# Kernel optimization log

Measured on AMD Instinct MI355X. Metric: run time of the kernel, lower is better.

Reference implementation:

```python
import jax, jax.numpy as jnp
import numpy as np

WS = 4          # window size per axis
HEADS = 3
HEAD_DIM = 32
DIM = 96
DISP = WS // 2  # displacement for shifted windows


def _make_mask(axis):
    # (w^3, w^3) additive mask, -inf across the wrap-around boundary on `axis`
    m = np.zeros((WS, WS, WS, WS, WS, WS), dtype=np.float32)
    d = DISP
    if axis == 0:
        m[-d:, :, :, :-d, :, :] = -np.inf
        m[:-d, :, :, -d:, :, :] = -np.inf
    elif axis == 1:
        m[:, -d:, :, :, :-d, :] = -np.inf
        m[:, :-d, :, :, -d:, :] = -np.inf
    else:
        m[:, :, -d:, :, :, :-d] = -np.inf
        m[:, :, :-d, :, :, -d:] = -np.inf
    return jnp.asarray(m.reshape(WS**3, WS**3))


def setup_inputs() -> dict:
    key = jax.random.key(0)
    k1, k2, k3, k4 = jax.random.split(key, 4)
    inner = HEADS * HEAD_DIM
    x = jax.random.normal(k1, (1, 64, 64, 64, DIM), dtype=jnp.float32)
    w_qkv = jax.random.normal(k2, (3 * inner, DIM), dtype=jnp.float32) * 0.02
    w_out = jax.random.normal(k3, (DIM, inner), dtype=jnp.float32) * 0.02
    b_out = jax.random.normal(k4, (DIM,), dtype=jnp.float32) * 0.02
    return {
        'x': x, 'w_qkv': w_qkv, 'w_out': w_out, 'b_out': b_out,
        'x_mask': _make_mask(0), 'y_mask': _make_mask(1), 'z_mask': _make_mask(2),
    }


def _forward(x, w_qkv, w_out, b_out, x_mask, y_mask, z_mask):
    scale = HEAD_DIM ** -0.5
    b, nx, ny, nz, _ = x.shape
    nwx, nwy, nwz = nx // WS, ny // WS, nz // WS
    seq = WS ** 3
    # cyclic shift by -displacement
    x = jnp.roll(x, shift=(-DISP, -DISP, -DISP), axis=(1, 2, 3))
    qkv = jnp.einsum('bxyzc,oc->bxyzo', x, w_qkv)
    q, k, v = jnp.split(qkv, 3, axis=-1)

    def win(t):  # -> (b, h, n_windows, seq, d)
        t = t.reshape(b, nwx, WS, nwy, WS, nwz, WS, HEADS, HEAD_DIM)
        t = t.transpose(0, 7, 1, 3, 5, 2, 4, 6, 8)
        return t.reshape(b, HEADS, nwx * nwy * nwz, seq, HEAD_DIM)

    q, k, v = win(q), win(k), win(v)
    dots = jnp.einsum('bhwid,bhwjd->bhwij', q, k) * scale

    # shifted-window masking (faithful to original einops relabeling, incl.
    # the final mislabeled rearrange which permutes the window grid)
    d = dots.reshape(b, HEADS, nwx, nwy, nwz, seq, seq)
    d = d.transpose(0, 1, 3, 4, 2, 5, 6)          # (b,h,ny,nz,nx,i,j)
    d = d.at[:, :, :, :, -1].add(x_mask)
    d = d.transpose(0, 1, 4, 3, 2, 5, 6)          # (b,h,nx,nz,ny,i,j)
    d = d.at[:, :, :, :, -1].add(y_mask)
    d = d.transpose(0, 1, 2, 4, 3, 5, 6)          # (b,h,nx,ny,nz,i,j)
    d = d.transpose(0, 1, 4, 2, 3, 5, 6)          # original's final rearrange bug
    dots = d.reshape(b, HEADS, nwx * nwy * nwz, seq, seq)

    attn = jax.nn.softmax(dots, axis=-1)
    out = jnp.einsum('bhwij,bhwjd->bhwid', attn, v)
    # un-window
    out = out.reshape(b, HEADS, nwx, nwy, nwz, WS, WS, WS, HEAD_DIM)
    out = out.transpose(0, 2, 5, 3, 6, 4, 7, 1, 8).reshape(b, nx, ny, nz, HEADS * HEAD_DIM)
    out = jnp.einsum('bxyzc,oc->bxyzo', out, w_out) + b_out
    # cyclic back shift
    return jnp.roll(out, shift=(DISP, DISP, DISP), axis=(1, 2, 3))


def reference(x, w_qkv, w_out, b_out, x_mask, y_mask, z_mask):
    return _forward(x, w_qkv, w_out, b_out, x_mask, y_mask, z_mask)
```

## Files before the change

kernel.cpp:

```cpp
#include <hip/hip_runtime.h>
#include <hip/hip_bf16.h>


using bf8   = __attribute__((ext_vector_type(8))) short;
using f32x4 = __attribute__((ext_vector_type(4))) float;

#define SQK 100
#define SP   68
#define SVT  72

__device__ __forceinline__ short f2b(float f) {
  __hip_bfloat16 h = __float2bfloat16(f);
  return *reinterpret_cast<short*>(&h);
}
__device__ __forceinline__ unsigned pk2(float a, float b) {
  return (unsigned)(unsigned short)f2b(a) | ((unsigned)(unsigned short)f2b(b) << 16);
}

__global__ void prep_weights(const float* __restrict__ wq, const float* __restrict__ wo,
                             short* __restrict__ wqb, short* __restrict__ wob) {
  int i = blockIdx.x * 256 + threadIdx.x;
  const float QS = 0.17677669529663687f;
  if (i < 288 * 96) wqb[i] = f2b(wq[i] * (i < 96 * 96 ? QS : 1.0f));
  if (i < 96 * 96)  wob[i] = f2b(wo[i]);
}

__device__ __forceinline__ void load_window_bf16(short* __restrict__ ys,
    const float* __restrict__ x, int wx, int wy, int wz, int tid) {
  #pragma unroll
  for (int it = 0; it < 6; ++it) {
    int idx = tid + it * 256;
    int s   = idx / 24;
    int c4  = (idx - s * 24) * 4;
    int sx = s >> 4, sy = (s >> 2) & 3, sz = s & 3;
    int gx = (wx * 4 + sx + 2) & 63;
    int gy = (wy * 4 + sy + 2) & 63;
    int gz = (wz * 4 + sz + 2) & 63;
    const float4 v = *reinterpret_cast<const float4*>(
        &x[(size_t)((gx * 64 + gy) * 64 + gz) * 96 + c4]);
    uint2 pk; pk.x = pk2(v.x, v.y); pk.y = pk2(v.z, v.w);
    *reinterpret_cast<uint2*>(&ys[s * SQK + c4]) = pk;
  }
}

__global__ __launch_bounds__(256, 3)
void fused_swin3d(const float* __restrict__ x,
                  const short* __restrict__ wqb,
                  const short* __restrict__ wob,
                  const float* __restrict__ bo,
                  float* __restrict__ out) {
  __shared__ short ls_q [64 * SQK];
  __shared__ short ls_k [64 * SQK];
  __shared__ short ls_vt[96 * SVT];
  __shared__ short ls_yp[64 * SQK];

  short* ys = ls_yp;
  short* lp = ls_yp;
  short* lo = ls_q;

  const int w  = blockIdx.x;
  const int p  = w >> 8, q = (w >> 4) & 15, r = w & 15;
  const int tid  = threadIdx.x;
  const int lane = tid & 63;
  const int wv   = tid >> 6;
  const int lr   = lane & 15;
  const int kg   = lane >> 4;
  const int arow  = wv * 16 + lr;
  const int drow0 = wv * 16 + kg * 4;

  load_window_bf16(ys, x, q, r, p, tid);
  __syncthreads();
  bf8 af0 = *reinterpret_cast<const bf8*>(&ys[arow * SQK +  0 + kg * 8]);
  bf8 af1 = *reinterpret_cast<const bf8*>(&ys[arow * SQK + 32 + kg * 8]);
  bf8 af2 = *reinterpret_cast<const bf8*>(&ys[arow * SQK + 64 + kg * 8]);
  #pragma unroll
  for (int n = 0; n < 12; ++n) {
    f32x4 acc = {0.f, 0.f, 0.f, 0.f};
    const short* wrow = &wqb[(n * 16 + lr) * 96 + kg * 8];
    acc = __builtin_amdgcn_mfma_f32_16x16x32_bf16(af0, *reinterpret_cast<const bf8*>(wrow +  0), acc, 0, 0, 0);
    acc = __builtin_amdgcn_mfma_f32_16x16x32_bf16(af1, *reinterpret_cast<const bf8*>(wrow + 32), acc, 0, 0, 0);
    acc = __builtin_amdgcn_mfma_f32_16x16x32_bf16(af2, *reinterpret_cast<const bf8*>(wrow + 64), acc, 0, 0, 0);
    short* dst = (n < 6) ? &ls_q[0] : &ls_k[0];
    const int nn = (n < 6) ? n : n - 6;
    #pragma unroll
    for (int ri = 0; ri < 4; ++ri)
      dst[(drow0 + ri) * SQK + nn * 16 + lr] = f2b(acc[ri]);
  }
  __syncthreads();

  load_window_bf16(ys, x, p, q, r, tid);
  __syncthreads();
  af0 = *reinterpret_cast<const bf8*>(&ys[arow * SQK +  0 + kg * 8]);
  af1 = *reinterpret_cast<const bf8*>(&ys[arow * SQK + 32 + kg * 8]);
  af2 = *reinterpret_cast<const bf8*>(&ys[arow * SQK + 64 + kg * 8]);
  #pragma unroll
  for (int n = 0; n < 6; ++n) {
    f32x4 acc = {0.f, 0.f, 0.f, 0.f};
    const short* wrow = &wqb[(192 + n * 16 + lr) * 96 + kg * 8];
    acc = __builtin_amdgcn_mfma_f32_16x16x32_bf16(af0, *reinterpret_cast<const bf8*>(wrow +  0), acc, 0, 0, 0);
    acc = __builtin_amdgcn_mfma_f32_16x16x32_bf16(af1, *reinterpret_cast<const bf8*>(wrow + 32), acc, 0, 0, 0);
    acc = __builtin_amdgcn_mfma_f32_16x16x32_bf16(af2, *reinterpret_cast<const bf8*>(wrow + 64), acc, 0, 0, 0);
    short4 vpk;
    vpk.x = f2b(acc[0]); vpk.y = f2b(acc[1]); vpk.z = f2b(acc[2]); vpk.w = f2b(acc[3]);
    *reinterpret_cast<short4*>(&ls_vt[(n * 16 + lr) * SVT + drow0]) = vpk;
  }
  __syncthreads();

  const bool mx = (q == 15), my = (r == 15);
  const bool ky = my && ((kg >= 2) != (lr >= 8));
  f32x4 acc_o[3][2];
  #pragma unroll
  for (int h = 0; h < 3; ++h)
    #pragma unroll
    for (int n = 0; n < 2; ++n)
      acc_o[h][n] = (f32x4){0.f, 0.f, 0.f, 0.f};

  #pragma unroll
  for (int h = 0; h < 3; ++h) {
    bf8 qa = *reinterpret_cast<const bf8*>(&ls_q[arow * SQK + h * 32 + kg * 8]);
    f32x4 sv[4];
    #pragma unroll
    for (int n = 0; n < 4; ++n) {
      bf8 kb = *reinterpret_cast<const bf8*>(&ls_k[(n * 16 + lr) * SQK + h * 32 + kg * 8]);
      f32x4 z = {0.f, 0.f, 0.f, 0.f};
      sv[n] = __builtin_amdgcn_mfma_f32_16x16x32_bf16(qa, kb, z, 0, 0, 0);
      const bool kill = ky || (mx && ((wv >= 2) != (n >= 2)));
      if (kill) sv[n] = (f32x4){-1e30f, -1e30f, -1e30f, -1e30f};
    }
    #pragma unroll
    for (int ri = 0; ri < 4; ++ri) {
      float s0 = sv[0][ri], s1 = sv[1][ri], s2 = sv[2][ri], s3 = sv[3][ri];
      float m = fmaxf(fmaxf(s0, s1), fmaxf(s2, s3));
      m = fmaxf(m, __shfl_xor(m, 1));
      m = fmaxf(m, __shfl_xor(m, 2));
      m = fmaxf(m, __shfl_xor(m, 4));
      m = fmaxf(m, __shfl_xor(m, 8));
      float e0 = __expf(s0 - m), e1 = __expf(s1 - m);
      float e2 = __expf(s2 - m), e3 = __expf(s3 - m);
      float sum = (e0 + e1) + (e2 + e3);
      sum += __shfl_xor(sum, 1);
      sum += __shfl_xor(sum, 2);
      sum += __shfl_xor(sum, 4);
      sum += __shfl_xor(sum, 8);
      const float inv = 1.f / sum;
      const int prow = (drow0 + ri) * SP;
      lp[prow +  0 + lr] = f2b(e0 * inv);
      lp[prow + 16 + lr] = f2b(e1 * inv);
      lp[prow + 32 + lr] = f2b(e2 * inv);
      lp[prow + 48 + lr] = f2b(e3 * inv);
    }
    #pragma unroll
    for (int t = 0; t < 2; ++t) {
      bf8 pa = *reinterpret_cast<const bf8*>(&lp[arow * SP + t * 32 + kg * 8]);
      #pragma unroll
      for (int n = 0; n < 2; ++n) {
        bf8 vb = *reinterpret_cast<const bf8*>(&ls_vt[(h * 32 + n * 16 + lr) * SVT + t * 32 + kg * 8]);
        acc_o[h][n] = __builtin_amdgcn_mfma_f32_16x16x32_bf16(pa, vb, acc_o[h][n], 0, 0, 0);
      }
    }
  }

  #pragma unroll
  for (int h = 0; h < 3; ++h)
    #pragma unroll
    for (int n = 0; n < 2; ++n)
      #pragma unroll
      for (int ri = 0; ri < 4; ++ri)
        lo[(drow0 + ri) * SQK + h * 32 + n * 16 + lr] = f2b(acc_o[h][n][ri]);

  bf8 oa0 = *reinterpret_cast<const bf8*>(&lo[arow * SQK +  0 + kg * 8]);
  bf8 oa1 = *reinterpret_cast<const bf8*>(&lo[arow * SQK + 32 + kg * 8]);
  bf8 oa2 = *reinterpret_cast<const bf8*>(&lo[arow * SQK + 64 + kg * 8]);

  float bias[6];
  #pragma unroll
  for (int n = 0; n < 6; ++n) bias[n] = bo[n * 16 + lr];

  size_t obase[4];
  #pragma unroll
  for (int ri = 0; ri < 4; ++ri) {
    const int s  = drow0 + ri;
    const int sx = s >> 4, sy = (s >> 2) & 3, sz = s & 3;
    const int gx = (p * 4 + sx + 2) & 63;
    const int gy = (q * 4 + sy + 2) & 63;
    const int gz = (r * 4 + sz + 2) & 63;
    obase[ri] = (size_t)((gx * 64 + gy) * 64 + gz) * 96;
  }
  #pragma unroll
  for (int n = 0; n < 6; ++n) {
    f32x4 acc = {0.f, 0.f, 0.f, 0.f};
    const short* wrow = &wob[(n * 16 + lr) * 96 + kg * 8];
    acc = __builtin_amdgcn_mfma_f32_16x16x32_bf16(oa0, *reinterpret_cast<const bf8*>(wrow +  0), acc, 0, 0, 0);
    acc = __builtin_amdgcn_mfma_f32_16x16x32_bf16(oa1, *reinterpret_cast<const bf8*>(wrow + 32), acc, 0, 0, 0);
    acc = __builtin_amdgcn_mfma_f32_16x16x32_bf16(oa2, *reinterpret_cast<const bf8*>(wrow + 64), acc, 0, 0, 0);
    #pragma unroll
    for (int ri = 0; ri < 4; ++ri)
      out[obase[ri] + n * 16 + lr] = acc[ri] + bias[n];
  }
}

extern "C" void kernel_launch(void* const* d_in, const int* in_sizes, int n_in,
                              void* d_out, int out_size, void* d_ws, size_t ws_size,
                              hipStream_t stream) {
  const float* x  = (const float*)d_in[0];
  const float* wq = (const float*)d_in[1];
  const float* wo = (const float*)d_in[2];
  const float* bo = (const float*)d_in[3];

  short* wqb = (short*)d_ws;
  short* wob = wqb + 288 * 96;

  prep_weights<<<(288 * 96 + 255) / 256, 256, 0, stream>>>(wq, wo, wqb, wob);
  fused_swin3d<<<4096, 256, 0, stream>>>(x, wqb, wob, bo, (float*)d_out);
}
```

Measured before the change: 108.8 us.

## Load x directly into MFMA fragments and transpose matmuls to drop staging LDS

Each thread now loads its input rows straight from global memory into registers as bf16 MFMA operands, so the LDS staging buffer and two barriers go away. All MFMAs swap their A/B operands, which puts results in a site-major layout. That lets results be written to LDS and to global output as packed short4/float4 vectors, and lets the softmax row sum be reduced with only two shuffles. The softmax drops max subtraction and writes zeros for masked entries directly. LDS usage shrinks and launch bounds rise to 4 blocks per CU, at the risk of more register pressure and exp overflow on large scores.

```diff
diff --git a/kernel.cpp b/kernel.cpp
--- a/kernel.cpp
+++ b/kernel.cpp
@@ -7,14 +7,21 @@
 
 #define SQK 100
 #define SP   68
-#define SVT  72
+#define SVT  68
 
 __device__ __forceinline__ short f2b(float f) {
   __hip_bfloat16 h = __float2bfloat16(f);
   return *reinterpret_cast<short*>(&h);
 }
-__device__ __forceinline__ unsigned pk2(float a, float b) {
-  return (unsigned)(unsigned short)f2b(a) | ((unsigned)(unsigned short)f2b(b) << 16);
+__device__ __forceinline__ short4 pk4(const f32x4& a) {
+  short4 s; s.x = f2b(a[0]); s.y = f2b(a[1]); s.z = f2b(a[2]); s.w = f2b(a[3]);
+  return s;
+}
+__device__ __forceinline__ bf8 cvt8(const float4& a, const float4& b) {
+  bf8 o;
+  o[0] = f2b(a.x); o[1] = f2b(a.y); o[2] = f2b(a.z); o[3] = f2b(a.w);
+  o[4] = f2b(b.x); o[5] = f2b(b.y); o[6] = f2b(b.z); o[7] = f2b(b.w);
+  return o;
 }
 
 __global__ void prep_weights(const float* __restrict__ wq, const float* __restrict__ wo,
@@ -25,38 +32,15 @@
   if (i < 96 * 96)  wob[i] = f2b(wo[i]);
 }
 
-__device__ __forceinline__ void load_window_bf16(short* __restrict__ ys,
-    const float* __restrict__ x, int wx, int wy, int wz, int tid) {
-  #pragma unroll
-  for (int it = 0; it < 6; ++it) {
-    int idx = tid + it * 256;
-    int s   = idx / 24;
-    int c4  = (idx - s * 24) * 4;
-    int sx = s >> 4, sy = (s >> 2) & 3, sz = s & 3;
-    int gx = (wx * 4 + sx + 2) & 63;
-    int gy = (wy * 4 + sy + 2) & 63;
-    int gz = (wz * 4 + sz + 2) & 63;
-    const float4 v = *reinterpret_cast<const float4*>(
-        &x[(size_t)((gx * 64 + gy) * 64 + gz) * 96 + c4]);
-    uint2 pk; pk.x = pk2(v.x, v.y); pk.y = pk2(v.z, v.w);
-    *reinterpret_cast<uint2*>(&ys[s * SQK + c4]) = pk;
-  }
-}
-
-__global__ __launch_bounds__(256, 3)
+__global__ __launch_bounds__(256, 4)
 void fused_swin3d(const float* __restrict__ x,
                   const short* __restrict__ wqb,
                   const short* __restrict__ wob,
                   const float* __restrict__ bo,
                   float* __restrict__ out) {
-  __shared__ short ls_q [64 * SQK];
-  __shared__ short ls_k [64 * SQK];
-  __shared__ short ls_vt[96 * SVT];
-  __shared__ short ls_yp[64 * SQK];
-
-  short* ys = ls_yp;
-  short* lp = ls_yp;
-  short* lo = ls_q;
+  __shared__ __align__(16) short ls_q [64 * SQK];
+  __shared__ __align__(16) short ls_k [64 * SQK];
+  __shared__ __align__(16) short ls_vt[96 * SVT];
 
   const int w  = blockIdx.x;
   const int p  = w >> 8, q = (w >> 4) & 15, r = w & 15;
@@ -65,98 +49,108 @@
   const int wv   = tid >> 6;
   const int lr   = lane & 15;
   const int kg   = lane >> 4;
-  const int arow  = wv * 16 + lr;
-  const int drow0 = wv * 16 + kg * 4;
+  const int site = wv * 16 + lr;
+  const int sy = (lr >> 2) & 3, sz = lr & 3;
+  const int ch0 = kg * 8;
 
-  load_window_bf16(ys, x, q, r, p, tid);
-  __syncthreads();
-  bf8 af0 = *reinterpret_cast<const bf8*>(&ys[arow * SQK +  0 + kg * 8]);
-  bf8 af1 = *reinterpret_cast<const bf8*>(&ys[arow * SQK + 32 + kg * 8]);
-  bf8 af2 = *reinterpret_cast<const bf8*>(&ys[arow * SQK + 64 + kg * 8]);
+  const int gx1 = (q * 4 + wv + 2) & 63, gy1 = (r * 4 + sy + 2) & 63, gz1 = (p * 4 + sz + 2) & 63;
+  const int gx2 = (p * 4 + wv + 2) & 63, gy2 = (q * 4 + sy + 2) & 63, gz2 = (r * 4 + sz + 2) & 63;
+  const size_t b1 = (size_t)((gx1 * 64 + gy1) * 64 + gz1) * 96;
+  const size_t b2 = (size_t)((gx2 * 64 + gy2) * 64 + gz2) * 96;
+
+  float4 xa[6], xb[6];
+  #pragma unroll
+  for (int f = 0; f < 3; ++f) {
+    xa[f]     = *reinterpret_cast<const float4*>(&x[b1 + f * 32 + ch0]);
+    xa[3 + f] = *reinterpret_cast<const float4*>(&x[b1 + f * 32 + ch0 + 4]);
+  }
+  #pragma unroll
+  for (int f = 0; f < 3; ++f) {
+    xb[f]     = *reinterpret_cast<const float4*>(&x[b2 + f * 32 + ch0]);
+    xb[3 + f] = *reinterpret_cast<const float4*>(&x[b2 + f * 32 + ch0 + 4]);
+  }
+  bf8 x1[3], x2[3];
+  #pragma unroll
+  for (int f = 0; f < 3; ++f) x1[f] = cvt8(xa[f], xa[3 + f]);
+
   #pragma unroll
   for (int n = 0; n < 12; ++n) {
     f32x4 acc = {0.f, 0.f, 0.f, 0.f};
-    const short* wrow = &wqb[(n * 16 + lr) * 96 + kg * 8];
-    acc = __builtin_amdgcn_mfma_f32_16x16x32_bf16(af0, *reinterpret_cast<const bf8*>(wrow +  0), acc, 0, 0, 0);
-    acc = __builtin_amdgcn_mfma_f32_16x16x32_bf16(af1, *reinterpret_cast<const bf8*>(wrow + 32), acc, 0, 0, 0);
-    acc = __builtin_amdgcn_mfma_f32_16x16x32_bf16(af2, *reinterpret_cast<const bf8*>(wrow + 64), acc, 0, 0, 0);
-    short* dst = (n < 6) ? &ls_q[0] : &ls_k[0];
+    const short* wrow = &wqb[(n * 16 + lr) * 96 + ch0];
+    acc = __builtin_amdgcn_mfma_f32_16x16x32_bf16(*reinterpret_cast<const bf8*>(wrow +  0), x1[0], acc, 0, 0, 0);
+    acc = __builtin_amdgcn_mfma_f32_16x16x32_bf16(*reinterpret_cast<const bf8*>(wrow + 32), x1[1], acc, 0, 0, 0);
+    acc = __builtin_amdgcn_mfma_f32_16x16x32_bf16(*reinterpret_cast<const bf8*>(wrow + 64), x1[2], acc, 0, 0, 0);
+    short* dst = (n < 6) ? ls_q : ls_k;
     const int nn = (n < 6) ? n : n - 6;
-    #pragma unroll
-    for (int ri = 0; ri < 4; ++ri)
-      dst[(drow0 + ri) * SQK + nn * 16 + lr] = f2b(acc[ri]);
+    *reinterpret_cast<short4*>(&dst[site * SQK + nn * 16 + kg * 4]) = pk4(acc);
+  }
+
+  #pragma unroll
+  for (int f = 0; f < 3; ++f) x2[f] = cvt8(xb[f], xb[3 + f]);
+  #pragma unroll
+  for (int n = 0; n < 6; ++n) {
+    f32x4 acc = {0.f, 0.f, 0.f, 0.f};
+    const short* wrow = &wqb[(192 + n * 16 + lr) * 96 + ch0];
+    acc = __builtin_amdgcn_mfma_f32_16x16x32_bf16(x2[0], *reinterpret_cast<const bf8*>(wrow +  0), acc, 0, 0, 0);
+    acc = __builtin_amdgcn_mfma_f32_16x16x32_bf16(x2[1], *reinterpret_cast<const bf8*>(wrow + 32), acc, 0, 0, 0);
+    acc = __builtin_amdgcn_mfma_f32_16x16x32_bf16(x2[2], *reinterpret_cast<const bf8*>(wrow + 64), acc, 0, 0, 0);
+    *reinterpret_cast<short4*>(&ls_vt[(n * 16 + lr) * SVT + wv * 16 + kg * 4]) = pk4(acc);
   }
   __syncthreads();
 
-  load_window_bf16(ys, x, p, q, r, tid);
-  __syncthreads();
-  af0 = *reinterpret_cast<const bf8*>(&ys[arow * SQK +  0 + kg * 8]);
-  af1 = *reinterpret_cast<const bf8*>(&ys[arow * SQK + 32 + kg * 8]);
-  af2 = *reinterpret_cast<const bf8*>(&ys[arow * SQK + 64 + kg * 8]);
-  #pragma unroll
-  for (int n = 0; n < 6; ++n) {
-    f32x4 acc = {0.f, 0.f, 0.f, 0.f};
-    const short* wrow = &wqb[(192 + n * 16 + lr) * 96 + kg * 8];
-    acc = __builtin_amdgcn_mfma_f32_16x16x32_bf16(af0, *reinterpret_cast<const bf8*>(wrow +  0), acc, 0, 0, 0);
-    acc = __builtin_amdgcn_mfma_f32_16x16x32_bf16(af1, *reinterpret_cast<const bf8*>(wrow + 32), acc, 0, 0, 0);
-    acc = __builtin_amdgcn_mfma_f32_16x16x32_bf16(af2, *reinterpret_cast<const bf8*>(wrow + 64), acc, 0, 0, 0);
-    short4 vpk;
-    vpk.x = f2b(acc[0]); vpk.y = f2b(acc[1]); vpk.z = f2b(acc[2]); vpk.w = f2b(acc[3]);
-    *reinterpret_cast<short4*>(&ls_vt[(n * 16 + lr) * SVT + drow0]) = vpk;
-  }
-  __syncthreads();
+  const bf8 qa0 = *reinterpret_cast<const bf8*>(&ls_q[site * SQK +  0 + ch0]);
+  const bf8 qa1 = *reinterpret_cast<const bf8*>(&ls_q[site * SQK + 32 + ch0]);
+  const bf8 qa2 = *reinterpret_cast<const bf8*>(&ls_q[site * SQK + 64 + ch0]);
 
   const bool mx = (q == 15), my = (r == 15);
-  const bool ky = my && ((kg >= 2) != (lr >= 8));
-  f32x4 acc_o[3][2];
+  const bool killy = my && ((lr >= 8) != (kg >= 2));
+  const int  pbase = wv * 16 * SQK + lr * SP;
+
+  f32x4 osw[3][2];
   #pragma unroll
   for (int h = 0; h < 3; ++h)
     #pragma unroll
-    for (int n = 0; n < 2; ++n)
-      acc_o[h][n] = (f32x4){0.f, 0.f, 0.f, 0.f};
+    for (int n = 0; n < 2; ++n) osw[h][n] = (f32x4){0.f, 0.f, 0.f, 0.f};
 
   #pragma unroll
   for (int h = 0; h < 3; ++h) {
-    bf8 qa = *reinterpret_cast<const bf8*>(&ls_q[arow * SQK + h * 32 + kg * 8]);
+    const bf8 qa = (h == 0) ? qa0 : (h == 1) ? qa1 : qa2;
     f32x4 sv[4];
     #pragma unroll
     for (int n = 0; n < 4; ++n) {
-      bf8 kb = *reinterpret_cast<const bf8*>(&ls_k[(n * 16 + lr) * SQK + h * 32 + kg * 8]);
+      bf8 kb = *reinterpret_cast<const bf8*>(&ls_k[(n * 16 + lr) * SQK + h * 32 + ch0]);
       f32x4 z = {0.f, 0.f, 0.f, 0.f};
-      sv[n] = __builtin_amdgcn_mfma_f32_16x16x32_bf16(qa, kb, z, 0, 0, 0);
-      const bool kill = ky || (mx && ((wv >= 2) != (n >= 2)));
-      if (kill) sv[n] = (f32x4){-1e30f, -1e30f, -1e30f, -1e30f};
+      sv[n] = __builtin_amdgcn_mfma_f32_16x16x32_bf16(kb, qa, z, 0, 0, 0);
     }
+    float e[16];
+    float sum = 0.f;
     #pragma unroll
-    for (int ri = 0; ri < 4; ++ri) {
-      float s0 = sv[0][ri], s1 = sv[1][ri], s2 = sv[2][ri], s3 = sv[3][ri];
-      float m = fmaxf(fmaxf(s0, s1), fmaxf(s2, s3));
-      m = fmaxf(m, __shfl_xor(m, 1));
-      m = fmaxf(m, __shfl_xor(m, 2));
-      m = fmaxf(m, __shfl_xor(m, 4));
-      m = fmaxf(m, __shfl_xor(m, 8));
-      float e0 = __expf(s0 - m), e1 = __expf(s1 - m);
-      float e2 = __expf(s2 - m), e3 = __expf(s3 - m);
-      float sum = (e0 + e1) + (e2 + e3);
-      sum += __shfl_xor(sum, 1);
-      sum += __shfl_xor(sum, 2);
-      sum += __shfl_xor(sum, 4);
-      sum += __shfl_xor(sum, 8);
-      const float inv = 1.f / sum;
-      const int prow = (drow0 + ri) * SP;
-      lp[prow +  0 + lr] = f2b(e0 * inv);
-      lp[prow + 16 + lr] = f2b(e1 * inv);
-      lp[prow + 32 + lr] = f2b(e2 * inv);
-      lp[prow + 48 + lr] = f2b(e3 * inv);
+    for (int n = 0; n < 4; ++n) {
+      const bool kill = killy || (mx && ((wv >= 2) != (n >= 2)));
+      #pragma unroll
+      for (int t = 0; t < 4; ++t) {
+        float ev = kill ? 0.f : __expf(sv[n][t]);
+        e[n * 4 + t] = ev;
+        sum += ev;
+      }
     }
+    sum += __shfl_xor(sum, 16);
+    sum += __shfl_xor(sum, 32);
+    const float inv = 1.f / sum;
     #pragma unroll
-    for (int t = 0; t < 2; ++t) {
-      bf8 pa = *reinterpret_cast<const bf8*>(&lp[arow * SP + t * 32 + kg * 8]);
-      #pragma unroll
-      for (int n = 0; n < 2; ++n) {
-        bf8 vb = *reinterpret_cast<const bf8*>(&ls_vt[(h * 32 + n * 16 + lr) * SVT + t * 32 + kg * 8]);
-        acc_o[h][n] = __builtin_amdgcn_mfma_f32_16x16x32_bf16(pa, vb, acc_o[h][n], 0, 0, 0);
-      }
+    for (int n = 0; n < 4; ++n) {
+      f32x4 ep = { e[n * 4 + 0] * inv, e[n * 4 + 1] * inv,
+                   e[n * 4 + 2] * inv, e[n * 4 + 3] * inv };
+      *reinterpret_cast<short4*>(&ls_q[pbase + n * 16 + kg * 4]) = pk4(ep);
+    }
+    const bf8 pa0 = *reinterpret_cast<const bf8*>(&ls_q[pbase +  0 + ch0]);
+    const bf8 pa1 = *reinterpret_cast<const bf8*>(&ls_q[pbase + 32 + ch0]);
+    #pragma unroll
+    for (int n = 0; n < 2; ++n) {
+      bf8 vb0 = *reinterpret_cast<const bf8*>(&ls_vt[(h * 32 + n * 16 + lr) * SVT +  0 + ch0]);
+      bf8 vb1 = *reinterpret_cast<const bf8*>(&ls_vt[(h * 32 + n * 16 + lr) * SVT + 32 + ch0]);
+      osw[h][n] = __builtin_amdgcn_mfma_f32_16x16x32_bf16(vb0, pa0, osw[h][n], 0, 0, 0);
+      osw[h][n] = __builtin_amdgcn_mfma_f32_16x16x32_bf16(vb1, pa1, osw[h][n], 0, 0, 0);
     }
   }
 
@@ -164,38 +158,24 @@
   for (int h = 0; h < 3; ++h)
     #pragma unroll
     for (int n = 0; n < 2; ++n)
-      #pragma unroll
-      for (int ri = 0; ri < 4; ++ri)
-        lo[(drow0 + ri) * SQK + h * 32 + n * 16 + lr] = f2b(acc_o[h][n][ri]);
+      *reinterpret_cast<short4*>(&ls_q[site * SQK + h * 32 + n * 16 + kg * 4]) = pk4(osw[h][n]);
 
-  bf8 oa0 = *reinterpret_cast<const bf8*>(&lo[arow * SQK +  0 + kg * 8]);
-  bf8 oa1 = *reinterpret_cast<const bf8*>(&lo[arow * SQK + 32 + kg * 8]);
-  bf8 oa2 = *reinterpret_cast<const bf8*>(&lo[arow * SQK + 64 + kg * 8]);
+  const bf8 oa0 = *reinterpret_cast<const bf8*>(&ls_q[site * SQK +  0 + ch0]);
+  const bf8 oa1 = *reinterpret_cast<const bf8*>(&ls_q[site * SQK + 32 + ch0]);
+  const bf8 oa2 = *reinterpret_cast<const bf8*>(&ls_q[site * SQK + 64 + ch0]);
 
-  float bias[6];
-  #pragma unroll
-  for (int n = 0; n < 6; ++n) bias[n] = bo[n * 16 + lr];
-
-  size_t obase[4];
-  #pragma unroll
-  for (int ri = 0; ri < 4; ++ri) {
-    const int s  = drow0 + ri;
-    const int sx = s >> 4, sy = (s >> 2) & 3, sz = s & 3;
-    const int gx = (p * 4 + sx + 2) & 63;
-    const int gy = (q * 4 + sy + 2) & 63;
-    const int gz = (r * 4 + sz + 2) & 63;
-    obase[ri] = (size_t)((gx * 64 + gy) * 64 + gz) * 96;
-  }
   #pragma unroll
   for (int n = 0; n < 6; ++n) {
     f32x4 acc = {0.f, 0.f, 0.f, 0.f};
-    const short* wrow = &wob[(n * 16 + lr) * 96 + kg * 8];
-    acc = __builtin_amdgcn_mfma_f32_16x16x32_bf16(oa0, *reinterpret_cast<const bf8*>(wrow +  0), acc, 0, 0, 0);
-    acc = __builtin_amdgcn_mfma_f32_16x16x32_bf16(oa1, *reinterpret_cast<const bf8*>(wrow + 32), acc, 0, 0, 0);
-    acc = __builtin_amdgcn_mfma_f32_16x16x32_bf16(oa2, *reinterpret_cast<const bf8*>(wrow + 64), acc, 0, 0, 0);
-    #pragma unroll
-    for (int ri = 0; ri < 4; ++ri)
-      out[obase[ri] + n * 16 + lr] = acc[ri] + bias[n];
+    const short* wrow = &wob[(n * 16 + lr) * 96 + ch0];
+    acc = __builtin_amdgcn_mfma_f32_16x16x32_bf16(*reinterpret_cast<const bf8*>(wrow +  0), oa0, acc, 0, 0, 0);
+    acc = __builtin_amdgcn_mfma_f32_16x16x32_bf16(*reinterpret_cast<const bf8*>(wrow + 32), oa1, acc, 0, 0, 0);
+    acc = __builtin_amdgcn_mfma_f32_16x16x32_bf16(*reinterpret_cast<const bf8*>(wrow + 64), oa2, acc, 0, 0, 0);
+    const float4 bb = *reinterpret_cast<const float4*>(&bo[n * 16 + kg * 4]);
+    float4 o4;
+    o4.x = acc[0] + bb.x; o4.y = acc[1] + bb.y;
+    o4.z = acc[2] + bb.z; o4.w = acc[3] + bb.w;
+    *reinterpret_cast<float4*>(&out[b2 + n * 16 + kg * 4]) = o4;
   }
 }
 
```

New measurement: 109.2 us. Within noise of the previous version (+0.4%).
